# Performance work log

Measured on AMD Instinct MI355X. Metric: run time of the kernel, lower is better.

Reference implementation:

```python
import jax, jax.numpy as jnp
import numpy as np

# Graph/batch constants (compressed-edge representation of graph.adjmat)
B, N, E, D = 64, 1024, 1_048_576, 128        # graphs, nodes/graph, edges, new_edge_dim
EDGE_DIM, MSSG_DIM, GLOB_DIM, CNDT_DIM = 64, 32, 8, 8
HIDDEN, N_HEADS = 256, 4
HEAD_DIM = D // N_HEADS                        # 32
ATTN_IN = MSSG_DIM + EDGE_DIM + GLOB_DIM + CNDT_DIM  # 112
NUM_SEG = B * N


def setup_inputs() -> dict:
    key = jax.random.key(0)
    ks = jax.random.split(key, 11)
    new_edges = jax.random.normal(ks[0], (E, D), dtype=jnp.float32)
    edges = jax.random.normal(ks[1], (E, EDGE_DIM), dtype=jnp.float32)
    pooled_mssgs = jax.random.normal(ks[2], (E, MSSG_DIM), dtype=jnp.float32)
    globs = jax.random.normal(ks[3], (B, GLOB_DIM), dtype=jnp.float32)
    cndts = jax.random.normal(ks[4], (B, CNDT_DIM), dtype=jnp.float32)
    W1 = jax.random.normal(ks[5], (ATTN_IN, HIDDEN), dtype=jnp.float32) * (1.0 / np.sqrt(ATTN_IN))
    b1 = jnp.zeros((HIDDEN,), dtype=jnp.float32)
    W2 = jax.random.normal(ks[6], (HIDDEN, N_HEADS), dtype=jnp.float32) * (1.0 / np.sqrt(HIDDEN))
    b2 = jnp.zeros((N_HEADS,), dtype=jnp.float32)
    batch_idx = jnp.sort(jax.random.randint(ks[7], (E,), 0, B, dtype=jnp.int32))
    recv_idx = jax.random.randint(ks[8], (E,), 0, N, dtype=jnp.int32)
    return dict(new_edges=new_edges, edges=edges, pooled_mssgs=pooled_mssgs,
                globs=globs, cndts=cndts, W1=W1, b1=b1, W2=W2, b2=b2,
                batch_idx=batch_idx, recv_idx=recv_idx)


def reference(new_edges, edges, pooled_mssgs, globs, cndts, W1, b1, W2, b2,
              batch_idx, recv_idx):
    # ctxt_from_mask: broadcast per-graph globs/cndts to each compressed edge  [E, g+c]
    ctxt = jnp.concatenate([globs[batch_idx], cndts[batch_idx]], axis=-1)
    # smart_cat([pooled_mssgs, graph.edges]) + ctxt concat inside DenseNetwork
    x = jnp.concatenate([pooled_mssgs, edges, ctxt], axis=-1)      # [E, 112]
    h = jax.nn.leaky_relu(x @ W1 + b1, 0.1)                        # [E, 256]
    logits = h @ W2 + b2                                           # [E, n_heads]

    # segment id = (graph, receiver) slot; adjmat nonzeros -> compressed edges
    seg = batch_idx * N + recv_idx                                 # [E]

    # aggr_via_sparse(..., reduction='softmax', dim=1): masked segment softmax per head
    m = jax.ops.segment_max(logits, seg, num_segments=NUM_SEG)     # [B*N, H]
    ex = jnp.exp(logits - m[seg])
    denom = jax.ops.segment_sum(ex, seg, num_segments=NUM_SEG)
    attn = ex / denom[seg]                                         # [E, H]

    # unsqueeze(-1).expand(-1,-1,head_dim).flatten(1) == repeat each head head_dim times
    w = jnp.repeat(attn, HEAD_DIM, axis=1)                         # [E, D]

    # aggr_via_sparse(..., 'sum', dim=1) then decompress onto dense [B, N, D]
    pooled = jax.ops.segment_sum(new_edges * w, seg, num_segments=NUM_SEG)
    return pooled.reshape(B, N, D)
```

## Files before the change

kernel.cpp:

```cpp
#include <hip/hip_runtime.h>
#include <hip/hip_bf16.h>
#include <cstdint>
#include <cstddef>

#define E_TOT   1048576
#define BGR     64
#define NN      1024
#define DD      128
#define HID     256
#define NH      4
#define NSEG    65536
#define KDIM    96
#define NKCH    12
#define BM      64
#define NTILES  (E_TOT/BM)
#define GRIDM   512
#define TPB     (NTILES/GRIDM)

typedef __attribute__((ext_vector_type(8))) short s16x8;
typedef __attribute__((ext_vector_type(4))) float f32x4;

static __device__ __forceinline__ unsigned short f2bf_rn(float f) {
    unsigned u = __float_as_uint(f);
    unsigned r = u + 0x7FFF + ((u >> 16) & 1);
    return (unsigned short)(r >> 16);
}

__global__ __launch_bounds__(256)
void k_misc(const float* __restrict__ W1, const float* __restrict__ b1,
            const float* __restrict__ globs, const float* __restrict__ cndts,
            const int* __restrict__ batch_idx, const int* __restrict__ recv_idx,
            short* __restrict__ Wg, float* __restrict__ ctxtc,
            int* __restrict__ counts)
{
    const int bid = blockIdx.x;
    const int tid = threadIdx.x;
    if (bid < 4096) {
        int e = bid * 256 + tid;
        atomicAdd(&counts[batch_idx[e] * NN + recv_idx[e]], 1);
    } else if (bid < 4096 + 96) {
        int idx = (bid - 4096) * 256 + tid;
        int kchunk = idx >> 11;
        int n      = (idx >> 3) & 255;
        int j      = idx & 7;
        int k      = kchunk * 8 + j;
        Wg[idx] = (short)f2bf_rn(W1[k * 256 + n]);
    } else {
        int b = bid - 4192, j = tid;
        float s = b1[j];
        #pragma unroll
        for (int g = 0; g < 8; ++g) s = fmaf(globs[b * 8 + g], W1[(96 + g) * 256 + j], s);
        #pragma unroll
        for (int c = 0; c < 8; ++c) s = fmaf(cndts[b * 8 + c], W1[(104 + c) * 256 + j], s);
        ctxtc[b * 256 + j] = s;
    }
}

__global__ __launch_bounds__(256)
void k_scan1(const int* __restrict__ counts, int* __restrict__ tmp_excl,
             int* __restrict__ blocksums)
{
    __shared__ int sh[256];
    const int t = threadIdx.x;
    const int gid = blockIdx.x * 256 + t;
    int c = counts[gid];
    sh[t] = c;
    __syncthreads();
    int v = c;
    for (int off = 1; off < 256; off <<= 1) {
        int u = (t >= off) ? sh[t - off] : 0;
        __syncthreads();
        v += u; sh[t] = v;
        __syncthreads();
    }
    tmp_excl[gid] = v - c;
    if (t == 255) blocksums[blockIdx.x] = v;
}

__global__ __launch_bounds__(256)
void k_scan3(const int* __restrict__ tmp_excl, const int* __restrict__ blocksums,
             int* __restrict__ offsets, int* __restrict__ cursor)
{
    __shared__ int swv[4];
    const int t = threadIdx.x;
    const int bid = blockIdx.x;
    int v = (t < bid) ? blocksums[t] : 0;
    #pragma unroll
    for (int off = 1; off < 64; off <<= 1) v += __shfl_xor(v, off);
    if ((t & 63) == 0) swv[t >> 6] = v;
    __syncthreads();
    const int base = swv[0] + swv[1] + swv[2] + swv[3];
    const int gid = bid * 256 + t;
    int o = tmp_excl[gid] + base;
    offsets[gid] = o;
    cursor[gid]  = o;
}

__global__ __launch_bounds__(512, 4)
void k_mlp_mfma(const float* __restrict__ pooled, const float* __restrict__ edges,
                const short* __restrict__ Wg,     const float* __restrict__ ctxtc,
                const float* __restrict__ W2,
                const int* __restrict__ batch_idx, const int* __restrict__ recv_idx,
                float* __restrict__ ex_out, float* __restrict__ denom,
                int* __restrict__ cursor, int* __restrict__ elist)
{
    __shared__ short Wl[NKCH * 256 * 8];
    __shared__ short Xl[NKCH * BM * 8];
    __shared__ float sW2[256 * 4];
    __shared__ float plog[4][BM][4];

    const int tid  = threadIdx.x;
    const int lane = tid & 63;
    const int wid  = tid >> 6;
    const int la   = lane & 15;
    const int g    = lane >> 4;
    const int es   = wid & 1;
    const int hq   = wid >> 1;

    {
        const float4* src = reinterpret_cast<const float4*>(Wg);
        float4* dst = reinterpret_cast<float4*>(Wl);
        #pragma unroll
        for (int i = 0; i < 6; ++i) dst[i * 512 + tid] = src[i * 512 + tid];
        if (tid < 256)
            *reinterpret_cast<float4*>(&sW2[tid * 4]) =
                reinterpret_cast<const float4*>(W2)[tid];
    }

    const int u0 = tid;
    const int u1 = tid + 512;
    const int e_u0 = u0 / 12, k_u0 = u0 - e_u0 * 12;
    const int e_u1 = u1 / 12, k_u1 = u1 - e_u1 * 12;

    {
        const int e0 = blockIdx.x * TPB * BM;
        {
            const int eg = e0 + e_u0;
            const float* p = (k_u0 < 4) ? (pooled + (size_t)eg * 32 + k_u0 * 8)
                                        : (edges + (size_t)eg * 64 + (k_u0 - 4) * 8);
            float4 v0 = reinterpret_cast<const float4*>(p)[0];
            float4 v1 = reinterpret_cast<const float4*>(p)[1];
            float vals[8] = {v0.x,v0.y,v0.z,v0.w,v1.x,v1.y,v1.z,v1.w};
            s16x8 hv;
            #pragma unroll
            for (int i = 0; i < 8; ++i) hv[i] = (short)f2bf_rn(vals[i]);
            *reinterpret_cast<s16x8*>(&Xl[(k_u0 * BM + e_u0) * 8]) = hv;
        }
        if (tid < 256) {
            const int eg = e0 + e_u1;
            const float* p = (k_u1 < 4) ? (pooled + (size_t)eg * 32 + k_u1 * 8)
                                        : (edges + (size_t)eg * 64 + (k_u1 - 4) * 8);
            float4 v0 = reinterpret_cast<const float4*>(p)[0];
            float4 v1 = reinterpret_cast<const float4*>(p)[1];
            float vals[8] = {v0.x,v0.y,v0.z,v0.w,v1.x,v1.y,v1.z,v1.w};
            s16x8 hv;
            #pragma unroll
            for (int i = 0; i < 8; ++i) hv[i] = (short)f2bf_rn(vals[i]);
            *reinterpret_cast<s16x8*>(&Xl[(k_u1 * BM + e_u1) * 8]) = hv;
        }
    }
    __syncthreads();

    for (int t = 0; t < TPB; ++t) {
        const int e0 = (blockIdx.x * TPB + t) * BM;
        const bool has_next = (t + 1 < TPB);

        float4 sa0, sa1, sb0, sb1;
        if (has_next) {
            const int en = e0 + BM;
            {
                const int eg = en + e_u0;
                const float* p = (k_u0 < 4) ? (pooled + (size_t)eg * 32 + k_u0 * 8)
                                            : (edges + (size_t)eg * 64 + (k_u0 - 4) * 8);
                sa0 = reinterpret_cast<const float4*>(p)[0];
                sa1 = reinterpret_cast<const float4*>(p)[1];
            }
            if (tid < 256) {
                const int eg = en + e_u1;
                const float* p = (k_u1 < 4) ? (pooled + (size_t)eg * 32 + k_u1 * 8)
                                            : (edges + (size_t)eg * 64 + (k_u1 - 4) * 8);
                sb0 = reinterpret_cast<const float4*>(p)[0];
                sb1 = reinterpret_cast<const float4*>(p)[1];
            }
        }

        f32x4 acc[4][2];
        #pragma unroll
        for (int i = 0; i < 4; ++i) {
            acc[i][0] = (f32x4){0.f, 0.f, 0.f, 0.f};
            acc[i][1] = (f32x4){0.f, 0.f, 0.f, 0.f};
        }
        #pragma unroll
        for (int ks = 0; ks < 3; ++ks) {
            const int kb = ks * 4 + g;
            const s16x8 xf0 = *reinterpret_cast<const s16x8*>(
                &Xl[(kb * BM + es * 32 + la) * 8]);
            const s16x8 xf1 = *reinterpret_cast<const s16x8*>(
                &Xl[(kb * BM + es * 32 + 16 + la) * 8]);
            const short* wrow = &Wl[(kb * 256 + hq * 64 + la) * 8];
            #pragma unroll
            for (int hf = 0; hf < 4; ++hf) {
                s16x8 wf = *reinterpret_cast<const s16x8*>(wrow + hf * 128);
                acc[hf][0] = __builtin_amdgcn_mfma_f32_16x16x32_bf16(wf, xf0, acc[hf][0], 0, 0, 0);
                acc[hf][1] = __builtin_amdgcn_mfma_f32_16x16x32_bf16(wf, xf1, acc[hf][1], 0, 0, 0);
            }
        }

        {
            const int ea = e0 + es * 32 + la;
            const int eb = ea + 16;
            const int ba = batch_idx[ea];
            const int bb = batch_idx[eb];
            const float* cxa_base = &ctxtc[(size_t)ba * 256 + hq * 64 + g * 4];
            const float* cxb_base = &ctxtc[(size_t)bb * 256 + hq * 64 + g * 4];
            float pa0 = 0.f, pa1 = 0.f, pa2 = 0.f, pa3 = 0.f;
            float pb0 = 0.f, pb1 = 0.f, pb2 = 0.f, pb3 = 0.f;
            #pragma unroll
            for (int hf = 0; hf < 4; ++hf) {
                const float4 cxa = *reinterpret_cast<const float4*>(cxa_base + hf * 16);
                const float4 cxb = *reinterpret_cast<const float4*>(cxb_base + hf * 16);
                const float cxaa[4] = {cxa.x, cxa.y, cxa.z, cxa.w};
                const float cxba[4] = {cxb.x, cxb.y, cxb.z, cxb.w};
                #pragma unroll
                for (int r = 0; r < 4; ++r) {
                    const int j = hq * 64 + hf * 16 + g * 4 + r;
                    const float4 w2v = *reinterpret_cast<const float4*>(&sW2[j * 4]);
                    float sa = acc[hf][0][r] + cxaa[r];
                    float ha = fmaxf(sa, 0.1f * sa);
                    float sb = acc[hf][1][r] + cxba[r];
                    float hb = fmaxf(sb, 0.1f * sb);
                    pa0 = fmaf(ha, w2v.x, pa0); pb0 = fmaf(hb, w2v.x, pb0);
                    pa1 = fmaf(ha, w2v.y, pa1); pb1 = fmaf(hb, w2v.y, pb1);
                    pa2 = fmaf(ha, w2v.z, pa2); pb2 = fmaf(hb, w2v.z, pb2);
                    pa3 = fmaf(ha, w2v.w, pa3); pb3 = fmaf(hb, w2v.w, pb3);
                }
            }
            pa0 += __shfl_xor(pa0, 16); pa0 += __shfl_xor(pa0, 32);
            pa1 += __shfl_xor(pa1, 16); pa1 += __shfl_xor(pa1, 32);
            pa2 += __shfl_xor(pa2, 16); pa2 += __shfl_xor(pa2, 32);
            pa3 += __shfl_xor(pa3, 16); pa3 += __shfl_xor(pa3, 32);
            pb0 += __shfl_xor(pb0, 16); pb0 += __shfl_xor(pb0, 32);
            pb1 += __shfl_xor(pb1, 16); pb1 += __shfl_xor(pb1, 32);
            pb2 += __shfl_xor(pb2, 16); pb2 += __shfl_xor(pb2, 32);
            pb3 += __shfl_xor(pb3, 16); pb3 += __shfl_xor(pb3, 32);
            float pla = (g == 0) ? pa0 : (g == 1) ? pa1 : (g == 2) ? pa2 : pa3;
            float plb = (g == 0) ? pb0 : (g == 1) ? pb1 : (g == 2) ? pb2 : pb3;
            plog[hq][es * 32 + la][g]      = pla;
            plog[hq][es * 32 + 16 + la][g] = plb;
        }
        __syncthreads();

        if (has_next) {
            {
                float vals[8] = {sa0.x,sa0.y,sa0.z,sa0.w,sa1.x,sa1.y,sa1.z,sa1.w};
                s16x8 hv;
                #pragma unroll
                for (int i = 0; i < 8; ++i) hv[i] = (short)f2bf_rn(vals[i]);
                *reinterpret_cast<s16x8*>(&Xl[(k_u0 * BM + e_u0) * 8]) = hv;
            }
            if (tid < 256) {
                float vals[8] = {sb0.x,sb0.y,sb0.z,sb0.w,sb1.x,sb1.y,sb1.z,sb1.w};
                s16x8 hv;
                #pragma unroll
                for (int i = 0; i < 8; ++i) hv[i] = (short)f2bf_rn(vals[i]);
                *reinterpret_cast<s16x8*>(&Xl[(k_u1 * BM + e_u1) * 8]) = hv;
            }
        }

        if (tid < 256) {
            const int e = tid >> 2;
            const int h = tid & 3;
            const int eg = e0 + e;
            float lg = plog[0][e][h] + plog[1][e][h] + plog[2][e][h] + plog[3][e][h];
            float exv = __expf(lg);
            ex_out[(size_t)eg * 4 + h] = exv;
            const int seg = batch_idx[eg] * NN + recv_idx[eg];
            atomicAdd(&denom[seg * 4 + h], exv);
            if (h == 0) {
                int pos = atomicAdd(&cursor[seg], 1);
                elist[pos] = eg;
            }
        }
        __syncthreads();
    }
}

__global__ __launch_bounds__(256)
void k_gather(const float* __restrict__ new_edges, const float* __restrict__ ex,
              const float* __restrict__ denom, const int* __restrict__ offsets,
              const int* __restrict__ counts, const int* __restrict__ elist,
              float* __restrict__ out)
{
    const int gid  = blockIdx.x * 256 + threadIdx.x;
    const int seg  = gid >> 6;
    const int lane = threadIdx.x & 63;
    if (seg >= NSEG) return;

    const int start = offsets[seg];
    const int cnt   = counts[seg];
    const int h     = lane >> 4;
    const int doff  = lane * 2;

    float a0 = 0.f, a1 = 0.f;
    int i = 0;
    for (; i + 4 <= cnt; i += 4) {
        const int el0 = elist[start + i + 0];
        const int el1 = elist[start + i + 1];
        const int el2 = elist[start + i + 2];
        const int el3 = elist[start + i + 3];
        const float w0 = ex[(size_t)el0 * 4 + h];
        const float w1 = ex[(size_t)el1 * 4 + h];
        const float w2 = ex[(size_t)el2 * 4 + h];
        const float w3 = ex[(size_t)el3 * 4 + h];
        const float2 n0 = *reinterpret_cast<const float2*>(new_edges + (size_t)el0 * DD + doff);
        const float2 n1 = *reinterpret_cast<const float2*>(new_edges + (size_t)el1 * DD + doff);
        const float2 n2 = *reinterpret_cast<const float2*>(new_edges + (size_t)el2 * DD + doff);
        const float2 n3 = *reinterpret_cast<const float2*>(new_edges + (size_t)el3 * DD + doff);
        a0 = fmaf(n0.x, w0, a0); a1 = fmaf(n0.y, w0, a1);
        a0 = fmaf(n1.x, w1, a0); a1 = fmaf(n1.y, w1, a1);
        a0 = fmaf(n2.x, w2, a0); a1 = fmaf(n2.y, w2, a1);
        a0 = fmaf(n3.x, w3, a0); a1 = fmaf(n3.y, w3, a1);
    }
    for (; i < cnt; ++i) {
        const int el = elist[start + i];
        const float w = ex[(size_t)el * 4 + h];
        const float2 n = *reinterpret_cast<const float2*>(new_edges + (size_t)el * DD + doff);
        a0 = fmaf(n.x, w, a0); a1 = fmaf(n.y, w, a1);
    }
    const float scale = (cnt > 0) ? 1.0f / denom[seg * 4 + h] : 0.0f;
    float2 r; r.x = a0 * scale; r.y = a1 * scale;
    *reinterpret_cast<float2*>(out + (size_t)seg * DD + doff) = r;
}

extern "C" void kernel_launch(void* const* d_in, const int* in_sizes, int n_in,
                              void* d_out, int out_size, void* d_ws, size_t ws_size,
                              hipStream_t stream)
{
    const float* new_edges = (const float*)d_in[0];
    const float* edges     = (const float*)d_in[1];
    const float* pooled    = (const float*)d_in[2];
    const float* globs     = (const float*)d_in[3];
    const float* cndts     = (const float*)d_in[4];
    const float* W1        = (const float*)d_in[5];
    const float* b1        = (const float*)d_in[6];
    const float* W2        = (const float*)d_in[7];
    const int*   batch_idx = (const int*)d_in[9];
    const int*   recv_idx  = (const int*)d_in[10];
    float* out = (float*)d_out;

    char* ws = (char*)d_ws;
    float* ex       = (float*)(ws);
    float* denom    = (float*)(ws + (size_t)16 * 1024 * 1024);
    char*  base17   = ws + (size_t)17 * 1024 * 1024;
    int*   counts   = (int*)(base17);
    int*   offs     = (int*)(base17 + 1 * 262144);
    int*   cursor   = (int*)(base17 + 2 * 262144);
    int*   tmp_excl = (int*)(base17 + 3 * 262144);
    int*   bsums    = (int*)(base17 + 4 * 262144);
    int*   elist    = (int*)(ws + (size_t)18 * 1024 * 1024);
    short* Wg       = (short*)(ws + (size_t)22 * 1024 * 1024);
    float* ctxtc    = (float*)(ws + (size_t)22 * 1024 * 1024 + 65536);

    hipMemsetAsync(denom, 0,
                   (size_t)NSEG * NH * sizeof(float) + (size_t)NSEG * sizeof(int),
                   stream);

    k_misc<<<4096 + 96 + 64, 256, 0, stream>>>(W1, b1, globs, cndts,
                                               batch_idx, recv_idx,
                                               Wg, ctxtc, counts);
    k_scan1<<<NSEG / 256, 256, 0, stream>>>(counts, tmp_excl, bsums);
    k_scan3<<<NSEG / 256, 256, 0, stream>>>(tmp_excl, bsums, offs, cursor);

    k_mlp_mfma<<<GRIDM, 512, 0, stream>>>(pooled, edges, Wg, ctxtc, W2,
                                          batch_idx, recv_idx, ex, denom,
                                          cursor, elist);

    k_gather<<<(NSEG * 64) / 256, 256, 0, stream>>>(new_edges, ex, denom,
                                                    offs, counts, elist, out);
}
```

Baseline: 325.6 us.

## Fuse scan passes via chained flags, vectorize histogram, add nontemporal loads

Replaces the two-pass exclusive scan with a single chained-scan kernel, where each block waits on its predecessor's published prefix through an acquire/release flag. The counting histogram now reads int4 indices and does four atomics per thread with a quarter of the blocks. The MLP and gather kernels switch to nontemporal loads and stores for streamed data, and the gather loop is unrolled by 8 to expose more memory-level parallelism. The chained scan relies on blocks being scheduled in order and serializes 256 blocks. The memset is widened to zero the flags.

```diff
diff --git a/kernel.cpp b/kernel.cpp
--- a/kernel.cpp
+++ b/kernel.cpp
@@ -19,6 +19,8 @@
 
 typedef __attribute__((ext_vector_type(8))) short s16x8;
 typedef __attribute__((ext_vector_type(4))) float f32x4;
+typedef __attribute__((ext_vector_type(4))) float f32x4v;
+typedef __attribute__((ext_vector_type(2))) float f32x2v;
 
 static __device__ __forceinline__ unsigned short f2bf_rn(float f) {
     unsigned u = __float_as_uint(f);
@@ -35,18 +37,23 @@
 {
     const int bid = blockIdx.x;
     const int tid = threadIdx.x;
-    if (bid < 4096) {
-        int e = bid * 256 + tid;
-        atomicAdd(&counts[batch_idx[e] * NN + recv_idx[e]], 1);
-    } else if (bid < 4096 + 96) {
-        int idx = (bid - 4096) * 256 + tid;
+    if (bid < 1024) {
+        int e4 = (bid * 256 + tid) * 4;
+        const int4 b4 = *reinterpret_cast<const int4*>(batch_idx + e4);
+        const int4 r4 = *reinterpret_cast<const int4*>(recv_idx + e4);
+        atomicAdd(&counts[b4.x * NN + r4.x], 1);
+        atomicAdd(&counts[b4.y * NN + r4.y], 1);
+        atomicAdd(&counts[b4.z * NN + r4.z], 1);
+        atomicAdd(&counts[b4.w * NN + r4.w], 1);
+    } else if (bid < 1024 + 96) {
+        int idx = (bid - 1024) * 256 + tid;
         int kchunk = idx >> 11;
         int n      = (idx >> 3) & 255;
         int j      = idx & 7;
         int k      = kchunk * 8 + j;
         Wg[idx] = (short)f2bf_rn(W1[k * 256 + n]);
     } else {
-        int b = bid - 4192, j = tid;
+        int b = bid - 1120, j = tid;
         float s = b1[j];
         #pragma unroll
         for (int g = 0; g < 8; ++g) s = fmaf(globs[b * 8 + g], W1[(96 + g) * 256 + j], s);
@@ -57,12 +64,14 @@
 }
 
 __global__ __launch_bounds__(256)
-void k_scan1(const int* __restrict__ counts, int* __restrict__ tmp_excl,
-             int* __restrict__ blocksums)
+void k_scan_chain(const int* __restrict__ counts, int* __restrict__ offsets,
+                  int* __restrict__ cursor, unsigned* __restrict__ flags)
 {
     __shared__ int sh[256];
+    __shared__ int sbase;
     const int t = threadIdx.x;
-    const int gid = blockIdx.x * 256 + t;
+    const int b = blockIdx.x;
+    const int gid = b * 256 + t;
     int c = counts[gid];
     sh[t] = c;
     __syncthreads();
@@ -73,25 +82,22 @@
         v += u; sh[t] = v;
         __syncthreads();
     }
-    tmp_excl[gid] = v - c;
-    if (t == 255) blocksums[blockIdx.x] = v;
-}
-
-__global__ __launch_bounds__(256)
-void k_scan3(const int* __restrict__ tmp_excl, const int* __restrict__ blocksums,
-             int* __restrict__ offsets, int* __restrict__ cursor)
-{
-    __shared__ int swv[4];
-    const int t = threadIdx.x;
-    const int bid = blockIdx.x;
-    int v = (t < bid) ? blocksums[t] : 0;
-    #pragma unroll
-    for (int off = 1; off < 64; off <<= 1) v += __shfl_xor(v, off);
-    if ((t & 63) == 0) swv[t >> 6] = v;
+    if (t == 0) {
+        int base = 0;
+        if (b > 0) {
+            unsigned p;
+            while ((p = __hip_atomic_load(&flags[b - 1], __ATOMIC_ACQUIRE,
+                                          __HIP_MEMORY_SCOPE_AGENT)) == 0u) {
+                __builtin_amdgcn_s_sleep(1);
+            }
+            base = (int)(p - 1u);
+        }
+        sbase = base;
+        __hip_atomic_store(&flags[b], (unsigned)(base + sh[255]) + 1u,
+                           __ATOMIC_RELEASE, __HIP_MEMORY_SCOPE_AGENT);
+    }
     __syncthreads();
-    const int base = swv[0] + swv[1] + swv[2] + swv[3];
-    const int gid = bid * 256 + t;
-    int o = tmp_excl[gid] + base;
+    const int o = sbase + v - c;
     offsets[gid] = o;
     cursor[gid]  = o;
 }
@@ -138,9 +144,9 @@
             const int eg = e0 + e_u0;
             const float* p = (k_u0 < 4) ? (pooled + (size_t)eg * 32 + k_u0 * 8)
                                         : (edges + (size_t)eg * 64 + (k_u0 - 4) * 8);
-            float4 v0 = reinterpret_cast<const float4*>(p)[0];
-            float4 v1 = reinterpret_cast<const float4*>(p)[1];
-            float vals[8] = {v0.x,v0.y,v0.z,v0.w,v1.x,v1.y,v1.z,v1.w};
+            f32x4v v0 = __builtin_nontemporal_load(reinterpret_cast<const f32x4v*>(p));
+            f32x4v v1 = __builtin_nontemporal_load(reinterpret_cast<const f32x4v*>(p) + 1);
+            float vals[8] = {v0[0],v0[1],v0[2],v0[3],v1[0],v1[1],v1[2],v1[3]};
             s16x8 hv;
             #pragma unroll
             for (int i = 0; i < 8; ++i) hv[i] = (short)f2bf_rn(vals[i]);
@@ -150,9 +156,9 @@
             const int eg = e0 + e_u1;
             const float* p = (k_u1 < 4) ? (pooled + (size_t)eg * 32 + k_u1 * 8)
                                         : (edges + (size_t)eg * 64 + (k_u1 - 4) * 8);
-            float4 v0 = reinterpret_cast<const float4*>(p)[0];
-            float4 v1 = reinterpret_cast<const float4*>(p)[1];
-            float vals[8] = {v0.x,v0.y,v0.z,v0.w,v1.x,v1.y,v1.z,v1.w};
+            f32x4v v0 = __builtin_nontemporal_load(reinterpret_cast<const f32x4v*>(p));
+            f32x4v v1 = __builtin_nontemporal_load(reinterpret_cast<const f32x4v*>(p) + 1);
+            float vals[8] = {v0[0],v0[1],v0[2],v0[3],v1[0],v1[1],v1[2],v1[3]};
             s16x8 hv;
             #pragma unroll
             for (int i = 0; i < 8; ++i) hv[i] = (short)f2bf_rn(vals[i]);
@@ -165,22 +171,22 @@
         const int e0 = (blockIdx.x * TPB + t) * BM;
         const bool has_next = (t + 1 < TPB);
 
-        float4 sa0, sa1, sb0, sb1;
+        f32x4v sa0, sa1, sb0, sb1;
         if (has_next) {
             const int en = e0 + BM;
             {
                 const int eg = en + e_u0;
                 const float* p = (k_u0 < 4) ? (pooled + (size_t)eg * 32 + k_u0 * 8)
                                             : (edges + (size_t)eg * 64 + (k_u0 - 4) * 8);
-                sa0 = reinterpret_cast<const float4*>(p)[0];
-                sa1 = reinterpret_cast<const float4*>(p)[1];
+                sa0 = __builtin_nontemporal_load(reinterpret_cast<const f32x4v*>(p));
+                sa1 = __builtin_nontemporal_load(reinterpret_cast<const f32x4v*>(p) + 1);
             }
             if (tid < 256) {
                 const int eg = en + e_u1;
                 const float* p = (k_u1 < 4) ? (pooled + (size_t)eg * 32 + k_u1 * 8)
                                             : (edges + (size_t)eg * 64 + (k_u1 - 4) * 8);
-                sb0 = reinterpret_cast<const float4*>(p)[0];
-                sb1 = reinterpret_cast<const float4*>(p)[1];
+                sb0 = __builtin_nontemporal_load(reinterpret_cast<const f32x4v*>(p));
+                sb1 = __builtin_nontemporal_load(reinterpret_cast<const f32x4v*>(p) + 1);
             }
         }
 
@@ -252,14 +258,14 @@
 
         if (has_next) {
             {
-                float vals[8] = {sa0.x,sa0.y,sa0.z,sa0.w,sa1.x,sa1.y,sa1.z,sa1.w};
+                float vals[8] = {sa0[0],sa0[1],sa0[2],sa0[3],sa1[0],sa1[1],sa1[2],sa1[3]};
                 s16x8 hv;
                 #pragma unroll
                 for (int i = 0; i < 8; ++i) hv[i] = (short)f2bf_rn(vals[i]);
                 *reinterpret_cast<s16x8*>(&Xl[(k_u0 * BM + e_u0) * 8]) = hv;
             }
             if (tid < 256) {
-                float vals[8] = {sb0.x,sb0.y,sb0.z,sb0.w,sb1.x,sb1.y,sb1.z,sb1.w};
+                float vals[8] = {sb0[0],sb0[1],sb0[2],sb0[3],sb1[0],sb1[1],sb1[2],sb1[3]};
                 s16x8 hv;
                 #pragma unroll
                 for (int i = 0; i < 8; ++i) hv[i] = (short)f2bf_rn(vals[i]);
@@ -303,6 +309,24 @@
 
     float a0 = 0.f, a1 = 0.f;
     int i = 0;
+    for (; i + 8 <= cnt; i += 8) {
+        int   el[8];
+        float w[8];
+        f32x2v n[8];
+        #pragma unroll
+        for (int u = 0; u < 8; ++u) el[u] = elist[start + i + u];
+        #pragma unroll
+        for (int u = 0; u < 8; ++u) {
+            w[u] = ex[(size_t)el[u] * 4 + h];
+            n[u] = __builtin_nontemporal_load(
+                reinterpret_cast<const f32x2v*>(new_edges + (size_t)el[u] * DD + doff));
+        }
+        #pragma unroll
+        for (int u = 0; u < 8; ++u) {
+            a0 = fmaf(n[u][0], w[u], a0);
+            a1 = fmaf(n[u][1], w[u], a1);
+        }
+    }
     for (; i + 4 <= cnt; i += 4) {
         const int el0 = elist[start + i + 0];
         const int el1 = elist[start + i + 1];
@@ -312,24 +336,30 @@
         const float w1 = ex[(size_t)el1 * 4 + h];
         const float w2 = ex[(size_t)el2 * 4 + h];
         const float w3 = ex[(size_t)el3 * 4 + h];
-        const float2 n0 = *reinterpret_cast<const float2*>(new_edges + (size_t)el0 * DD + doff);
-        const float2 n1 = *reinterpret_cast<const float2*>(new_edges + (size_t)el1 * DD + doff);
-        const float2 n2 = *reinterpret_cast<const float2*>(new_edges + (size_t)el2 * DD + doff);
-        const float2 n3 = *reinterpret_cast<const float2*>(new_edges + (size_t)el3 * DD + doff);
-        a0 = fmaf(n0.x, w0, a0); a1 = fmaf(n0.y, w0, a1);
-        a0 = fmaf(n1.x, w1, a0); a1 = fmaf(n1.y, w1, a1);
-        a0 = fmaf(n2.x, w2, a0); a1 = fmaf(n2.y, w2, a1);
-        a0 = fmaf(n3.x, w3, a0); a1 = fmaf(n3.y, w3, a1);
+        const f32x2v n0 = __builtin_nontemporal_load(
+            reinterpret_cast<const f32x2v*>(new_edges + (size_t)el0 * DD + doff));
+        const f32x2v n1 = __builtin_nontemporal_load(
+            reinterpret_cast<const f32x2v*>(new_edges + (size_t)el1 * DD + doff));
+        const f32x2v n2 = __builtin_nontemporal_load(
+            reinterpret_cast<const f32x2v*>(new_edges + (size_t)el2 * DD + doff));
+        const f32x2v n3 = __builtin_nontemporal_load(
+            reinterpret_cast<const f32x2v*>(new_edges + (size_t)el3 * DD + doff));
+        a0 = fmaf(n0[0], w0, a0); a1 = fmaf(n0[1], w0, a1);
+        a0 = fmaf(n1[0], w1, a0); a1 = fmaf(n1[1], w1, a1);
+        a0 = fmaf(n2[0], w2, a0); a1 = fmaf(n2[1], w2, a1);
+        a0 = fmaf(n3[0], w3, a0); a1 = fmaf(n3[1], w3, a1);
     }
     for (; i < cnt; ++i) {
         const int el = elist[start + i];
         const float w = ex[(size_t)el * 4 + h];
-        const float2 n = *reinterpret_cast<const float2*>(new_edges + (size_t)el * DD + doff);
-        a0 = fmaf(n.x, w, a0); a1 = fmaf(n.y, w, a1);
+        const f32x2v n = __builtin_nontemporal_load(
+            reinterpret_cast<const f32x2v*>(new_edges + (size_t)el * DD + doff));
+        a0 = fmaf(n[0], w, a0); a1 = fmaf(n[1], w, a1);
     }
     const float scale = (cnt > 0) ? 1.0f / denom[seg * 4 + h] : 0.0f;
-    float2 r; r.x = a0 * scale; r.y = a1 * scale;
-    *reinterpret_cast<float2*>(out + (size_t)seg * DD + doff) = r;
+    f32x2v r; r[0] = a0 * scale; r[1] = a1 * scale;
+    __builtin_nontemporal_store(r,
+        reinterpret_cast<f32x2v*>(out + (size_t)seg * DD + doff));
 }
 
 extern "C" void kernel_launch(void* const* d_in, const int* in_sizes, int n_in,
@@ -349,27 +379,25 @@
     float* out = (float*)d_out;
 
     char* ws = (char*)d_ws;
-    float* ex       = (float*)(ws);
-    float* denom    = (float*)(ws + (size_t)16 * 1024 * 1024);
-    char*  base17   = ws + (size_t)17 * 1024 * 1024;
-    int*   counts   = (int*)(base17);
-    int*   offs     = (int*)(base17 + 1 * 262144);
-    int*   cursor   = (int*)(base17 + 2 * 262144);
-    int*   tmp_excl = (int*)(base17 + 3 * 262144);
-    int*   bsums    = (int*)(base17 + 4 * 262144);
-    int*   elist    = (int*)(ws + (size_t)18 * 1024 * 1024);
-    short* Wg       = (short*)(ws + (size_t)22 * 1024 * 1024);
-    float* ctxtc    = (float*)(ws + (size_t)22 * 1024 * 1024 + 65536);
+    float*    ex     = (float*)(ws);
+    float*    denom  = (float*)(ws + (size_t)16 * 1024 * 1024);
+    char*     base17 = ws + (size_t)17 * 1024 * 1024;
+    int*      counts = (int*)(base17);
+    unsigned* flags  = (unsigned*)(base17 + 262144);
+    int*      offs   = (int*)(base17 + 262144 + 4096);
+    int*      cursor = (int*)(base17 + 2 * 262144 + 4096);
+    int*      elist  = (int*)(ws + (size_t)18 * 1024 * 1024);
+    short*    Wg     = (short*)(ws + (size_t)22 * 1024 * 1024);
+    float*    ctxtc  = (float*)(ws + (size_t)22 * 1024 * 1024 + 65536);
 
     hipMemsetAsync(denom, 0,
-                   (size_t)NSEG * NH * sizeof(float) + (size_t)NSEG * sizeof(int),
-                   stream);
-
-    k_misc<<<4096 + 96 + 64, 256, 0, stream>>>(W1, b1, globs, cndts,
+                   (size_t)NSEG * NH * sizeof(float) + (size_t)NSEG * sizeof(int)
+                   + 4096, stream);
+
+    k_misc<<<1024 + 96 + 64, 256, 0, stream>>>(W1, b1, globs, cndts,
                                                batch_idx, recv_idx,
                                                Wg, ctxtc, counts);
-    k_scan1<<<NSEG / 256, 256, 0, stream>>>(counts, tmp_excl, bsums);
-    k_scan3<<<NSEG / 256, 256, 0, stream>>>(tmp_excl, bsums, offs, cursor);
+    k_scan_chain<<<NSEG / 256, 256, 0, stream>>>(counts, offs, cursor, flags);
 
     k_mlp_mfma<<<GRIDM, 512, 0, stream>>>(pooled, edges, Wg, ctxtc, W2,
                                           batch_idx, recv_idx, ex, denom,
```

Result: slower. 974.6 us (+199.3%).
